# Kernel tuning notes

Hardware: AMD Instinct MI355X
Metric: run time of the kernel (lower is better)

The kernel has to match this reference:

```python
import jax, jax.numpy as jnp
import numpy as np

T, B, D = 2048, 16, 1024


def setup_inputs() -> dict:
    key = jax.random.key(0)
    ks = jax.random.split(key, 8)
    std = 1.0 / D ** 0.5
    x = jax.random.normal(ks[0], (T, B, D), dtype=jnp.float32)
    h0 = jnp.zeros((B, D), dtype=jnp.float32)
    Wx = jax.random.uniform(ks[1], (D, D), jnp.float32, -std, std)
    R = jax.random.uniform(ks[2], (D, D), jnp.float32, -std, std)
    bias = jnp.zeros((D,), dtype=jnp.float32)
    W_delta = jax.random.uniform(ks[3], (D, D), jnp.float32, -std * 0.1, std * 0.1)
    b_delta = jnp.full((D,), 3.0, dtype=jnp.float32)  # delta_init
    A = jax.random.uniform(ks[4], (D,), jnp.float32, -0.5, 0.5)  # A_init_range
    W_gate_x = jax.random.uniform(ks[5], (D, D), jnp.float32, -std, std)
    W_gate_h = jax.random.uniform(ks[6], (D, D), jnp.float32, -std, std)
    b_gate = jnp.zeros((D,), dtype=jnp.float32)
    return {"x": x, "h0": h0, "Wx": Wx, "R": R, "bias": bias,
            "W_delta": W_delta, "b_delta": b_delta, "A": A,
            "W_gate_x": W_gate_x, "W_gate_h": W_gate_h, "b_gate": b_gate}


def reference(x, h0, Wx, R, bias, W_delta, b_delta, A, W_gate_x, W_gate_h, b_gate):
    # Input-dependent timestep: dt = softplus(x @ W_delta^T + b_delta), [T,B,D]
    dt = jax.nn.softplus(jnp.einsum('tbd,ed->tbe', x, W_delta) + b_delta)
    # Mamba-style log parameterization: decay_rate in (0,1), alpha in (0,1)
    decay_rate = jnp.exp(-jnp.exp(A))                 # [D]
    alpha = jnp.exp(-dt * decay_rate)                 # [T,B,D]
    # Precompute input projection once (big GEMM outside the scan)
    wx = jnp.einsum('tbd,ed->tbe', x, Wx) + bias      # [T,B,D]

    def step(h, inp):
        wx_t, a_t = inp                               # [B,D], [B,D]
        cand = jnp.tanh(h @ R.T + wx_t)               # nonlinear candidate
        h_new = a_t * h + (1.0 - a_t) * cand          # exponential blend
        return h_new, h_new

    _, h_out = jax.lax.scan(step, h0, (wx, alpha))    # h_out: [T,B,D] == h[1:]

    # h+x selective output gate
    gate_raw = (jnp.einsum('tbd,ed->tbe', x, W_gate_x)
                + jnp.einsum('tbd,ed->tbe', h_out, W_gate_h) + b_gate)
    return h_out * jax.nn.silu(gate_raw)
```

## Files before the change

### kernel.cpp

```cpp
#include <hip/hip_runtime.h>
#include <cstdint>
#include <cstddef>

typedef _Float16 f16;
typedef _Float16 f16x8 __attribute__((ext_vector_type(8)));
typedef _Float16 f16x4v __attribute__((ext_vector_type(4)));
typedef float f32x4 __attribute__((ext_vector_type(4)));
typedef unsigned uint2v __attribute__((ext_vector_type(2)));

#define TT 2048
#define BB 16
#define DD 1024
#define MM (TT*BB)
#define LDST 40
#define FPAD 16

__global__ void cvt_kernel(const float* __restrict__ in, f16* __restrict__ out, int n4){
  int stride = gridDim.x * blockDim.x;
  for (int j = blockIdx.x*blockDim.x + threadIdx.x; j < n4; j += stride){
    float4 v = ((const float4*)in)[j];
    f16x4v o;
    o[0]=(f16)v.x; o[1]=(f16)v.y; o[2]=(f16)v.z; o[3]=(f16)v.w;
    ((f16x4v*)out)[j] = o;
  }
}

__global__ void init_rec_kernel(const float* __restrict__ h0, f16* __restrict__ hbuf,
                                unsigned* __restrict__ flags){
  int tid = blockIdx.x*blockDim.x + threadIdx.x;
  if (tid < 64*FPAD) flags[tid] = 0u;
  if (tid < BB*DD) hbuf[tid] = (f16)h0[tid];
}

__global__ __launch_bounds__(256)
void gemm_f16_kernel(const f16* __restrict__ A, const f16* __restrict__ Bw,
                     float* __restrict__ out32, f16* __restrict__ out16,
                     const float* __restrict__ vec1, const float* __restrict__ vec2,
                     const f16* __restrict__ gxin, int epi)
{
  __shared__ f16 As[128*LDST];
  __shared__ f16 Bs[128*LDST];
  const int K = DD;
  int tid = threadIdx.x;
  int l = tid & 63, w = tid >> 6;
  int wr = w >> 1, wc = w & 1;
  int bm = blockIdx.x, bn = blockIdx.y;

  f32x4 acc[4][4];
  #pragma unroll
  for (int i=0;i<4;++i)
    #pragma unroll
    for (int j=0;j<4;++j)
      acc[i][j] = (f32x4){0.f,0.f,0.f,0.f};

  const int r0 = tid >> 2;
  const int q  = tid & 3;

  for (int kt = 0; kt < K/32; ++kt){
    __syncthreads();
    #pragma unroll
    for (int hh=0; hh<2; ++hh){
      int row = hh*64 + r0;
      uint4 va = *(const uint4*)(A  + (size_t)(bm*128+row)*K + kt*32 + q*8);
      uint4 vb = *(const uint4*)(Bw + (size_t)(bn*128+row)*K + kt*32 + q*8);
      *(uint4*)(As + row*LDST + q*8) = va;
      *(uint4*)(Bs + row*LDST + q*8) = vb;
    }
    __syncthreads();
    int lr = l & 15, kg = (l >> 4) * 8;
    f16x8 af[4], bf[4];
    #pragma unroll
    for (int i=0;i<4;++i){
      af[i] = *(const f16x8*)(As + (wr*64 + i*16 + lr)*LDST + kg);
      bf[i] = *(const f16x8*)(Bs + (wc*64 + i*16 + lr)*LDST + kg);
    }
    #pragma unroll
    for (int i=0;i<4;++i)
      #pragma unroll
      for (int j=0;j<4;++j)
        acc[i][j] = __builtin_amdgcn_mfma_f32_16x16x32_f16(af[i], bf[j], acc[i][j], 0,0,0);
  }

  int lr = l & 15, lh = l >> 4;
  #pragma unroll
  for (int i=0;i<4;++i){
    #pragma unroll
    for (int j=0;j<4;++j){
      #pragma unroll
      for (int r=0;r<4;++r){
        int row = bm*128 + wr*64 + i*16 + lh*4 + r;
        int col = bn*128 + wc*64 + j*16 + lr;
        float v = acc[i][j][r];
        size_t off = (size_t)row*DD + col;
        if (epi == 0){
          out32[off] = v + vec1[col];
        } else if (epi == 1){
          float pre = v + vec1[col];
          float sp  = (pre > 20.f) ? pre : log1pf(expf(pre));
          float decay = expf(-expf(vec2[col]));
          out32[off] = expf(-sp*decay);
        } else if (epi == 2){
          out16[off] = (f16)(v + vec1[col]);
        } else {
          float g = v + (float)gxin[off];
          float hval = (float)A[off];
          out32[off] = hval * g / (1.f + expf(-g));
        }
      }
    }
  }
}

__global__ __launch_bounds__(64)
void rec_kernel(const f16* __restrict__ Rf, const float* __restrict__ wx,
                const float* __restrict__ alpha, const float* __restrict__ h0,
                f16* __restrict__ hbuf, f16* __restrict__ hout,
                unsigned* __restrict__ flags)
{
  __shared__ f16 Rlds[32*64*8];

  int l = threadIdx.x;
  int j = blockIdx.x;
  int e0 = j * 16;

  #pragma unroll
  for (int kt=0; kt<32; ++kt){
    int e = e0 + (l & 15);
    int d = kt*32 + (l >> 4)*8;
    *(uint4*)(Rlds + ((size_t)kt*64 + l)*8) = *(const uint4*)(Rf + (size_t)e*DD + d);
  }

  int b = l & 15, rr0 = (l >> 4) * 4;
  float4 hstate = *(const float4*)(h0 + (size_t)b*DD + e0 + rr0);
  __syncthreads();

  f32x4 wxv = *(const f32x4*)(wx + (size_t)b*DD + e0 + rr0);
  f32x4 alv = *(const f32x4*)(alpha + (size_t)b*DD + e0 + rr0);

  for (int t = 0; t < TT; ++t){
    if (t > 0){
      const unsigned* fp = flags + l*FPAD;
      int guard = 0;
      unsigned long long notready = 1ull;
      while (notready && guard < 2000000){
        unsigned fv = __hip_atomic_load(fp, __ATOMIC_RELAXED, __HIP_MEMORY_SCOPE_AGENT);
        notready = __ballot(fv < (unsigned)t);
        ++guard;
        if (notready) __builtin_amdgcn_s_sleep(1);
      }
    }

    const f16* hb = hbuf + (size_t)(t & 1) * (BB*DD);
    f16x8 hfr[32];
    #pragma unroll
    for (int kt=0; kt<32; ++kt){
      const f16* hp = hb + (size_t)b*DD + kt*32 + (l >> 4)*8;
      asm volatile("global_load_dwordx4 %0, %1, off sc0 sc1"
                   : "=v"(hfr[kt]) : "v"(hp) : "memory");
    }
    asm volatile("s_waitcnt vmcnt(0)" ::: "memory");
    __builtin_amdgcn_sched_barrier(0);

    int tn = (t+1 < TT) ? (t+1) : t;
    size_t offn = ((size_t)tn*BB + b)*DD + e0 + rr0;
    f32x4 wxn = *(const f32x4*)(wx + offn);
    f32x4 aln = *(const f32x4*)(alpha + offn);

    f32x4 acc = (f32x4){0.f,0.f,0.f,0.f};
    #pragma unroll
    for (int kt=0; kt<32; ++kt){
      f16x8 a = *(const f16x8*)(Rlds + ((size_t)kt*64 + l)*8);
      acc = __builtin_amdgcn_mfma_f32_16x16x32_f16(a, hfr[kt], acc, 0, 0, 0);
    }

    f16x4v h4;
    float hs[4] = {hstate.x, hstate.y, hstate.z, hstate.w};
    #pragma unroll
    for (int r=0;r<4;++r){
      float z = acc[r] + wxv[r];
      float cand = tanhf(z);
      float hn = alv[r]*hs[r] + (1.f - alv[r])*cand;
      hs[r] = hn;
      h4[r] = (f16)hn;
    }
    hstate = (float4){hs[0], hs[1], hs[2], hs[3]};

    f16* hw = hbuf + (size_t)((t+1) & 1) * (BB*DD) + (size_t)b*DD + e0 + rr0;
    uint2v hv = __builtin_bit_cast(uint2v, h4);
    asm volatile("global_store_dwordx2 %0, %1, off sc0 sc1"
                 :: "v"(hw), "v"(hv) : "memory");
    asm volatile("s_waitcnt vmcnt(0)" ::: "memory");
    if (l == 0)
      __hip_atomic_store(flags + j*FPAD, (unsigned)(t+1),
                         __ATOMIC_RELAXED, __HIP_MEMORY_SCOPE_AGENT);

    *(f16x4v*)(hout + ((size_t)t*BB + b)*DD + e0 + rr0) = h4;
    wxv = wxn; alv = aln;
  }
}

extern "C" void kernel_launch(void* const* d_in, const int* in_sizes, int n_in,
                              void* d_out, int out_size, void* d_ws, size_t ws_size,
                              hipStream_t stream)
{
  const float* x    = (const float*)d_in[0];
  const float* h0   = (const float*)d_in[1];
  const float* Wx   = (const float*)d_in[2];
  const float* R    = (const float*)d_in[3];
  const float* bias = (const float*)d_in[4];
  const float* Wd   = (const float*)d_in[5];
  const float* bd   = (const float*)d_in[6];
  const float* Aar  = (const float*)d_in[7];
  const float* Wgx  = (const float*)d_in[8];
  const float* Wgh  = (const float*)d_in[9];
  const float* bg   = (const float*)d_in[10];
  float* out = (float*)d_out;

  char* ws = (char*)d_ws;
  size_t off = 0;
  auto carve = [&](size_t bytes) -> void* {
    void* p = ws + off;
    off += (bytes + 255) & ~(size_t)255;
    return p;
  };
  f16* x16    = (f16*)carve((size_t)MM*DD*2);
  f16* Wx16   = (f16*)carve((size_t)DD*DD*2);
  f16* Wd16   = (f16*)carve((size_t)DD*DD*2);
  f16* Wgx16  = (f16*)carve((size_t)DD*DD*2);
  f16* Wgh16  = (f16*)carve((size_t)DD*DD*2);
  f16* R16    = (f16*)carve((size_t)DD*DD*2);
  float* alphaB = (float*)carve((size_t)MM*DD*4);
  f16* gx16   = (f16*)carve((size_t)MM*DD*2);
  f16* hout16 = (f16*)carve((size_t)MM*DD*2);
  f16* hbuf   = (f16*)carve((size_t)2*BB*DD*2);
  unsigned* flags = (unsigned*)carve(64*FPAD*4);
  if (off > ws_size) return;

  float* wxbuf = out;

  cvt_kernel<<<1024, 256, 0, stream>>>(x,   x16,   MM*DD/4);
  cvt_kernel<<<256,  256, 0, stream>>>(Wx,  Wx16,  DD*DD/4);
  cvt_kernel<<<256,  256, 0, stream>>>(Wd,  Wd16,  DD*DD/4);
  cvt_kernel<<<256,  256, 0, stream>>>(Wgx, Wgx16, DD*DD/4);
  cvt_kernel<<<256,  256, 0, stream>>>(Wgh, Wgh16, DD*DD/4);
  cvt_kernel<<<256,  256, 0, stream>>>(R,   R16,   DD*DD/4);
  init_rec_kernel<<<64, 256, 0, stream>>>(h0, hbuf, flags);

  dim3 gg(MM/128, DD/128);
  gemm_f16_kernel<<<gg, 256, 0, stream>>>(x16, Wx16,  wxbuf,  nullptr, bias, nullptr, nullptr, 0);
  gemm_f16_kernel<<<gg, 256, 0, stream>>>(x16, Wd16,  alphaB, nullptr, bd,   Aar,     nullptr, 1);
  gemm_f16_kernel<<<gg, 256, 0, stream>>>(x16, Wgx16, nullptr, gx16,   bg,   nullptr, nullptr, 2);

  rec_kernel<<<64, 64, 0, stream>>>(R16, wxbuf, alphaB, h0, hbuf, hout16, flags);

  gemm_f16_kernel<<<gg, 256, 0, stream>>>(hout16, Wgh16, out, nullptr, nullptr, nullptr, gx16, 3);
}
```

Measured before the change: 7.577 ms.

## Store wx/alpha in fp16, split recurrence MFMA chain, fuse weight conversions

The wx and alpha GEMM epilogues now write fp16 instead of fp32, halving their store traffic and the recurrence kernel's per-step loads. In the recurrence, MFMAs for the first half of K start once half of the h loads have landed, and use four independent accumulators to break the dependent MFMA chain. The five weight conversion launches are merged into a single 2D-grid kernel. Storing alpha in fp16 near 1 loses precision in the decay and may raise error over the long recurrence.

```diff
diff --git a/kernel.cpp b/kernel.cpp
--- a/kernel.cpp
+++ b/kernel.cpp
@@ -23,6 +23,23 @@
     o[0]=(f16)v.x; o[1]=(f16)v.y; o[2]=(f16)v.z; o[3]=(f16)v.w;
     ((f16x4v*)out)[j] = o;
   }
+}
+
+__global__ void cvt5_kernel(const float* __restrict__ a0, const float* __restrict__ a1,
+                            const float* __restrict__ a2, const float* __restrict__ a3,
+                            const float* __restrict__ a4,
+                            f16* __restrict__ o0, f16* __restrict__ o1,
+                            f16* __restrict__ o2, f16* __restrict__ o3, f16* __restrict__ o4){
+  const float* src[5] = {a0,a1,a2,a3,a4};
+  f16* dst[5] = {o0,o1,o2,o3,o4};
+  int which = blockIdx.y;
+  const float* in = src[which];
+  f16* out = dst[which];
+  int j = blockIdx.x*blockDim.x + threadIdx.x;
+  float4 v = ((const float4*)in)[j];
+  f16x4v o;
+  o[0]=(f16)v.x; o[1]=(f16)v.y; o[2]=(f16)v.z; o[3]=(f16)v.w;
+  ((f16x4v*)out)[j] = o;
 }
 
 __global__ void init_rec_kernel(const float* __restrict__ h0, f16* __restrict__ hbuf,
@@ -93,12 +110,12 @@
         float v = acc[i][j][r];
         size_t off = (size_t)row*DD + col;
         if (epi == 0){
-          out32[off] = v + vec1[col];
+          out16[off] = (f16)(v + vec1[col]);
         } else if (epi == 1){
           float pre = v + vec1[col];
           float sp  = (pre > 20.f) ? pre : log1pf(expf(pre));
           float decay = expf(-expf(vec2[col]));
-          out32[off] = expf(-sp*decay);
+          out16[off] = (f16)expf(-sp*decay);
         } else if (epi == 2){
           out16[off] = (f16)(v + vec1[col]);
         } else {
@@ -112,8 +129,8 @@
 }
 
 __global__ __launch_bounds__(64)
-void rec_kernel(const f16* __restrict__ Rf, const float* __restrict__ wx,
-                const float* __restrict__ alpha, const float* __restrict__ h0,
+void rec_kernel(const f16* __restrict__ Rf, const f16* __restrict__ wx,
+                const f16* __restrict__ alpha, const float* __restrict__ h0,
                 f16* __restrict__ hbuf, f16* __restrict__ hout,
                 unsigned* __restrict__ flags)
 {
@@ -134,8 +151,13 @@
   float4 hstate = *(const float4*)(h0 + (size_t)b*DD + e0 + rr0);
   __syncthreads();
 
-  f32x4 wxv = *(const f32x4*)(wx + (size_t)b*DD + e0 + rr0);
-  f32x4 alv = *(const f32x4*)(alpha + (size_t)b*DD + e0 + rr0);
+  f32x4 wxv, alv;
+  {
+    f16x4v wh = *(const f16x4v*)(wx + (size_t)b*DD + e0 + rr0);
+    f16x4v ah = *(const f16x4v*)(alpha + (size_t)b*DD + e0 + rr0);
+    #pragma unroll
+    for (int r=0;r<4;++r){ wxv[r] = (float)wh[r]; alv[r] = (float)ah[r]; }
+  }
 
   for (int t = 0; t < TT; ++t){
     if (t > 0){
@@ -158,20 +180,32 @@
       asm volatile("global_load_dwordx4 %0, %1, off sc0 sc1"
                    : "=v"(hfr[kt]) : "v"(hp) : "memory");
     }
+
+    f32x4 accv[4];
+    #pragma unroll
+    for (int c=0;c<4;++c) accv[c] = (f32x4){0.f,0.f,0.f,0.f};
+
+    asm volatile("s_waitcnt vmcnt(16)" ::: "memory");
+    __builtin_amdgcn_sched_barrier(0);
+    #pragma unroll
+    for (int kt=0; kt<16; ++kt){
+      f16x8 a = *(const f16x8*)(Rlds + ((size_t)kt*64 + l)*8);
+      accv[kt&3] = __builtin_amdgcn_mfma_f32_16x16x32_f16(a, hfr[kt], accv[kt&3], 0, 0, 0);
+    }
     asm volatile("s_waitcnt vmcnt(0)" ::: "memory");
     __builtin_amdgcn_sched_barrier(0);
 
     int tn = (t+1 < TT) ? (t+1) : t;
     size_t offn = ((size_t)tn*BB + b)*DD + e0 + rr0;
-    f32x4 wxn = *(const f32x4*)(wx + offn);
-    f32x4 aln = *(const f32x4*)(alpha + offn);
-
-    f32x4 acc = (f32x4){0.f,0.f,0.f,0.f};
-    #pragma unroll
-    for (int kt=0; kt<32; ++kt){
+    f16x4v whn = *(const f16x4v*)(wx + offn);
+    f16x4v ahn = *(const f16x4v*)(alpha + offn);
+
+    #pragma unroll
+    for (int kt=16; kt<32; ++kt){
       f16x8 a = *(const f16x8*)(Rlds + ((size_t)kt*64 + l)*8);
-      acc = __builtin_amdgcn_mfma_f32_16x16x32_f16(a, hfr[kt], acc, 0, 0, 0);
-    }
+      accv[kt&3] = __builtin_amdgcn_mfma_f32_16x16x32_f16(a, hfr[kt], accv[kt&3], 0, 0, 0);
+    }
+    f32x4 acc = (accv[0]+accv[1]) + (accv[2]+accv[3]);
 
     f16x4v h4;
     float hs[4] = {hstate.x, hstate.y, hstate.z, hstate.w};
@@ -195,7 +229,8 @@
                          __ATOMIC_RELAXED, __HIP_MEMORY_SCOPE_AGENT);
 
     *(f16x4v*)(hout + ((size_t)t*BB + b)*DD + e0 + rr0) = h4;
-    wxv = wxn; alv = aln;
+    #pragma unroll
+    for (int r=0;r<4;++r){ wxv[r] = (float)whn[r]; alv[r] = (float)ahn[r]; }
   }
 }
 
@@ -229,29 +264,26 @@
   f16* Wgx16  = (f16*)carve((size_t)DD*DD*2);
   f16* Wgh16  = (f16*)carve((size_t)DD*DD*2);
   f16* R16    = (f16*)carve((size_t)DD*DD*2);
-  float* alphaB = (float*)carve((size_t)MM*DD*4);
+  f16* wx16   = (f16*)carve((size_t)MM*DD*2);
+  f16* al16   = (f16*)carve((size_t)MM*DD*2);
   f16* gx16   = (f16*)carve((size_t)MM*DD*2);
   f16* hout16 = (f16*)carve((size_t)MM*DD*2);
   f16* hbuf   = (f16*)carve((size_t)2*BB*DD*2);
   unsigned* flags = (unsigned*)carve(64*FPAD*4);
   if (off > ws_size) return;
 
-  float* wxbuf = out;
-
-  cvt_kernel<<<1024, 256, 0, stream>>>(x,   x16,   MM*DD/4);
-  cvt_kernel<<<256,  256, 0, stream>>>(Wx,  Wx16,  DD*DD/4);
-  cvt_kernel<<<256,  256, 0, stream>>>(Wd,  Wd16,  DD*DD/4);
-  cvt_kernel<<<256,  256, 0, stream>>>(Wgx, Wgx16, DD*DD/4);
-  cvt_kernel<<<256,  256, 0, stream>>>(Wgh, Wgh16, DD*DD/4);
-  cvt_kernel<<<256,  256, 0, stream>>>(R,   R16,   DD*DD/4);
+  cvt_kernel<<<1024, 256, 0, stream>>>(x, x16, MM*DD/4);
+  dim3 g5(DD*DD/4/256, 5);
+  cvt5_kernel<<<g5, 256, 0, stream>>>(Wx, Wd, Wgx, Wgh, R,
+                                      Wx16, Wd16, Wgx16, Wgh16, R16);
   init_rec_kernel<<<64, 256, 0, stream>>>(h0, hbuf, flags);
 
   dim3 gg(MM/128, DD/128);
-  gemm_f16_kernel<<<gg, 256, 0, stream>>>(x16, Wx16,  wxbuf,  nullptr, bias, nullptr, nullptr, 0);
-  gemm_f16_kernel<<<gg, 256, 0, stream>>>(x16, Wd16,  alphaB, nullptr, bd,   Aar,     nullptr, 1);
-  gemm_f16_kernel<<<gg, 256, 0, stream>>>(x16, Wgx16, nullptr, gx16,   bg,   nullptr, nullptr, 2);
-
-  rec_kernel<<<64, 64, 0, stream>>>(R16, wxbuf, alphaB, h0, hbuf, hout16, flags);
+  gemm_f16_kernel<<<gg, 256, 0, stream>>>(x16, Wx16,  nullptr, wx16, bias, nullptr, nullptr, 0);
+  gemm_f16_kernel<<<gg, 256, 0, stream>>>(x16, Wd16,  nullptr, al16, bd,   Aar,     nullptr, 1);
+  gemm_f16_kernel<<<gg, 256, 0, stream>>>(x16, Wgx16, nullptr, gx16, bg,   nullptr, nullptr, 2);
+
+  rec_kernel<<<64, 64, 0, stream>>>(R16, wx16, al16, h0, hbuf, hout16, flags);
 
   gemm_f16_kernel<<<gg, 256, 0, stream>>>(hout16, Wgh16, out, nullptr, nullptr, nullptr, gx16, 3);
 }
```

New measurement: 7.280 ms. -3.9%, faster.
